# Kernel tuning notes

Measured on AMD Instinct MI355X. Metric: run time of the kernel, lower is better.

## Reference

```python
import jax, jax.numpy as jnp
import numpy as np

N = 50000      # nodes
E = 800000     # edges (before self-loops)
DIN = 256
HID = 64
HEADS = 4
DOUT = 128
NEG_SLOPE = 0.2  # PyG GATConv default leaky-relu slope


def setup_inputs() -> dict:
    key = jax.random.key(0)
    ks = jax.random.split(key, 10)
    s = 0.05
    x = jax.random.normal(ks[0], (N, DIN), jnp.float32)
    edge_index = jax.random.randint(ks[1], (2, E), 0, N, dtype=jnp.int32)
    W1 = jax.random.normal(ks[2], (DIN, HEADS * HID), jnp.float32) * s
    a1_src = jax.random.normal(ks[3], (HEADS, HID), jnp.float32) * s
    a1_dst = jax.random.normal(ks[4], (HEADS, HID), jnp.float32) * s
    b1 = jnp.zeros((HEADS * HID,), jnp.float32)
    W2 = jax.random.normal(ks[5], (HEADS * HID, DOUT), jnp.float32) * s
    a2_src = jax.random.normal(ks[6], (1, DOUT), jnp.float32) * s
    a2_dst = jax.random.normal(ks[7], (1, DOUT), jnp.float32) * s
    b2 = jnp.zeros((DOUT,), jnp.float32)
    return {"x": x, "edge_index": edge_index,
            "W1": W1, "a1_src": a1_src, "a1_dst": a1_dst, "b1": b1,
            "W2": W2, "a2_src": a2_src, "a2_dst": a2_dst, "b2": b2}


def _gat_conv(x, src, dst, W, a_src, a_dst, b, heads, concat):
    """PyG-style GATConv (self-loops already appended to src/dst)."""
    n = x.shape[0]
    h = (x @ W).reshape(n, heads, -1)               # [N, H, C]
    e_src = jnp.einsum('nhc,hc->nh', h, a_src)       # [N, H]
    e_dst = jnp.einsum('nhc,hc->nh', h, a_dst)
    logits = jax.nn.leaky_relu(e_src[src] + e_dst[dst], NEG_SLOPE)  # [E', H]
    # segment softmax over incoming edges of each dst node
    m = jax.ops.segment_max(logits, dst, num_segments=n)
    ex = jnp.exp(logits - m[dst])
    denom = jax.ops.segment_sum(ex, dst, num_segments=n)
    alpha = ex / (denom[dst] + 1e-16)                # [E', H]
    msg = alpha[:, :, None] * h[src]                 # [E', H, C]
    out = jax.ops.segment_sum(msg, dst, num_segments=n)  # [N, H, C]
    if concat:
        out = out.reshape(n, -1)
    else:
        out = out.mean(axis=1)
    return out + b


def reference(x, edge_index, W1, a1_src, a1_dst, b1, W2, a2_src, a2_dst, b2):
    n = x.shape[0]
    loop = jnp.arange(n, dtype=edge_index.dtype)
    src = jnp.concatenate([edge_index[0], loop])
    dst = jnp.concatenate([edge_index[1], loop])
    h = jax.nn.elu(_gat_conv(x, src, dst, W1, a1_src, a1_dst, b1, HEADS, True))
    h = jax.nn.elu(_gat_conv(h, src, dst, W2, a2_src, a2_dst, b2, 1, False))
    return h.mean(axis=1)  # [N]
```

## Files before the change

kernel.cpp:

```cpp
#include <hip/hip_runtime.h>
#include <math.h>

#define N_NODES 50000
#define M_PAD   50048
#define N_EDGES 800000
#define EP (N_EDGES + N_NODES)
#define DIN 256
#define HEADS 4
#define HID 64
#define F1 256
#define F2 128
#define NEG_SLOPE 0.2f
#define SCAN_NBLK ((N_NODES + 255)/256)
#define HIST_NB ((EP + 255)/256)
#define SA_NB (M_PAD*F1/4/256)
#define WT_TOT (DIN*F1 + F1*F2)
#define WT_NB ((WT_TOT + 255)/256)

typedef short bf16x8 __attribute__((ext_vector_type(8)));
typedef float f32x4  __attribute__((ext_vector_type(4)));

static __device__ __forceinline__ float leaky(float x){ return x > 0.f ? x : NEG_SLOPE*x; }
static __device__ __forceinline__ float elu_f(float x){ return x > 0.f ? x : (__expf(x)-1.f); }
static __device__ __forceinline__ float b2f(unsigned short u){ return __uint_as_float(((unsigned)u)<<16); }
static __device__ __forceinline__ unsigned short f2b(float f){
  unsigned u = __float_as_uint(f);
  return (unsigned short)((u + 0x7fffu + ((u>>16)&1u)) >> 16);
}

__global__ __launch_bounds__(256) void k_prep(const float* __restrict__ X, unsigned short* __restrict__ Ahi,
    const float* __restrict__ W1, const float* __restrict__ W2,
    unsigned short* __restrict__ Bt1, unsigned short* __restrict__ Bt2,
    const int* __restrict__ dst, int* __restrict__ counts){
  unsigned b = blockIdx.x;
  if (b < SA_NB){
    int gid = b*256 + threadIdx.x;
    size_t base = (size_t)gid*4;
    int row = (int)(base >> 8);
    ushort4 hi;
    if (row < N_NODES){
      float4 v = *(const float4*)(X + base);
      hi.x=f2b(v.x); hi.y=f2b(v.y); hi.z=f2b(v.z); hi.w=f2b(v.w);
    } else {
      hi = {0,0,0,0};
    }
    *(ushort4*)(Ahi + base) = hi;
  } else if (b < SA_NB + WT_NB){
    int t = (b - SA_NB)*256 + threadIdx.x;
    if (t < DIN*F1){
      int n = t / DIN, k = t % DIN;
      Bt1[(unsigned)n*DIN + k] = f2b(W1[(unsigned)k*F1 + n]);
    } else if (t < WT_TOT){
      int u = t - DIN*F1;
      int n = u / F1, k = u % F1;
      Bt2[(unsigned)n*F1 + k] = f2b(W2[(unsigned)k*F2 + n]);
    }
  } else {
    int e = (b - SA_NB - WT_NB)*256 + threadIdx.x;
    if (e < EP){
      int d = (e < N_EDGES) ? dst[e] : (e - N_EDGES);
      atomicAdd(&counts[d], 1);
    }
  }
}

__global__ __launch_bounds__(256) void k_scan1(const int* __restrict__ counts,
                                               int* __restrict__ exc, int* __restrict__ bsum){
  int i = blockIdx.x*256 + threadIdx.x;
  int v = (i < N_NODES) ? counts[i] : 0;
  int lane = threadIdx.x & 63, wave = threadIdx.x >> 6;
  int inc = v;
  #pragma unroll
  for (int off=1; off<64; off<<=1){
    int n = __shfl_up(inc, off);
    if (lane >= off) inc += n;
  }
  __shared__ int wsum[4];
  if (lane == 63) wsum[wave] = inc;
  __syncthreads();
  int wpre = 0;
  #pragma unroll
  for (int w=0; w<4; w++) if (w < wave) wpre += wsum[w];
  if (i < N_NODES) exc[i] = wpre + inc - v;
  if (threadIdx.x == 255) bsum[blockIdx.x] = wpre + inc;
}

__global__ __launch_bounds__(256) void k_scan3d(const int* __restrict__ exc, const int* __restrict__ bsum,
                                                const int* __restrict__ counts,
                                                int* __restrict__ offsets, int* __restrict__ cursor,
                                                int* __restrict__ dbin, int* __restrict__ bcount){
  int t = threadIdx.x;
  int lane = t & 63, wave = t >> 6;
  int v = (t < (int)blockIdx.x) ? bsum[t] : 0;
  #pragma unroll
  for (int off=1; off<64; off<<=1) v += __shfl_xor(v, off);
  __shared__ int ws[4];
  __shared__ int hh[256];
  if (lane == 0) ws[wave] = v;
  hh[t] = 0;
  __syncthreads();
  int bpref = ws[0] + ws[1] + ws[2] + ws[3];
  int i = blockIdx.x*256 + t;
  if (i < N_NODES){
    int o = exc[i] + bpref;
    offsets[i] = o;
    cursor[i] = o;
    int b = counts[i]; if (b > 255) b = 255;
    atomicAdd(&hh[b], 1);
  }
  if (i == 0) offsets[N_NODES] = EP;
  __syncthreads();
  int c = hh[t];
  bcount[(unsigned)blockIdx.x*256 + t] = c;
  if (c) atomicAdd(&dbin[t], c);
}

__global__ __launch_bounds__(256) void k_scatter_dcol(const int* __restrict__ src, const int* __restrict__ dst,
                          int* __restrict__ cursor, int* __restrict__ sorted_src, int* __restrict__ sorted_dst,
                          const int* __restrict__ dbin, const int* __restrict__ bcount, int* __restrict__ colbase){
  if (blockIdx.x < HIST_NB){
    int e = blockIdx.x*256 + threadIdx.x;
    if (e >= EP) return;
    int s, d;
    if (e < N_EDGES){ s = src[e]; d = dst[e]; } else { s = d = e - N_EDGES; }
    int pos = atomicAdd(&cursor[d], 1);
    sorted_src[pos] = s;
    sorted_dst[pos] = d;
  } else {
    int i = threadIdx.x;
    int v = dbin[i];
    int lane = i & 63, wave = i >> 6;
    int inc = v;
    #pragma unroll
    for (int off=1; off<64; off<<=1){
      int n = __shfl_up(inc, off);
      if (lane >= off) inc += n;
    }
    __shared__ int wsum[4];
    if (lane == 63) wsum[wave] = inc;
    __syncthreads();
    int wpre = 0;
    #pragma unroll
    for (int w=0; w<4; w++) if (w < wave) wpre += wsum[w];
    int run = wpre + inc - v;
    for (int blk=0; blk<SCAN_NBLK; blk++){
      colbase[(unsigned)blk*256 + i] = run;
      run += bcount[(unsigned)blk*256 + i];
    }
  }
}

__global__ __launch_bounds__(256) void k_dscatter(const int* __restrict__ counts, const int* __restrict__ colbase,
                                                  int* __restrict__ perm){
  __shared__ int h[256];
  h[threadIdx.x] = 0;
  __syncthreads();
  int i = blockIdx.x*256 + threadIdx.x;
  if (i < N_NODES){
    int b = counts[i]; if (b > 255) b = 255;
    int r = atomicAdd(&h[b], 1);
    perm[colbase[(unsigned)blockIdx.x*256 + b] + r] = i;
  }
}

__global__ __launch_bounds__(256) void k_gemm1f(
    const unsigned short* __restrict__ A, const unsigned short* __restrict__ Bt,
    const float* __restrict__ a1s, const float* __restrict__ a1d,
    unsigned short* __restrict__ Cbf, float* __restrict__ es, float* __restrict__ ed){
  const int K = 256, Nc = F1;
  int tid = threadIdx.x;
  int wave = tid>>6, lane = tid&63;
  int wc = wave;
  int row0 = blockIdx.x*64;
  int col0 = wc*64;
  int lrow = lane&15, lk = (lane>>4)*8;
  f32x4 acc[4][4] = {};
  bf16x8 aA[4], bA[4], aB[4], bB[4];
  auto LOADF = [&](bf16x8* av, bf16x8* bv, int KS){
    #pragma unroll
    for (int i=0;i<4;i++){
      av[i] = *(const bf16x8*)(A  + (unsigned)(row0 + i*16 + lrow)*K + KS + lk);
      bv[i] = *(const bf16x8*)(Bt + (unsigned)(col0 + i*16 + lrow)*K + KS + lk);
    }
  };
  auto MFMAS = [&](bf16x8* av, bf16x8* bv){
    #pragma unroll
    for (int i=0;i<4;i++)
      #pragma unroll
      for (int j=0;j<4;j++)
        acc[i][j] = __builtin_amdgcn_mfma_f32_16x16x32_bf16(av[i], bv[j], acc[i][j], 0,0,0);
  };
  LOADF(aA,bA,0);
  #pragma unroll
  for (int ks=0; ks<K; ks+=64){
    LOADF(aB,bB,ks+32);
    MFMAS(aA,bA);
    if (ks+64 < K) LOADF(aA,bA,ks+64);
    MFMAS(aB,bB);
  }
  int crow = (lane>>4)*4, ccol = lane&15;
  #pragma unroll
  for (int i=0;i<4;i++)
    #pragma unroll
    for (int j=0;j<4;j++)
      #pragma unroll
      for (int q=0;q<4;q++){
        int r = row0 + i*16 + crow + q;
        int c = col0 + j*16 + ccol;
        Cbf[(unsigned)r*Nc + c] = f2b(acc[i][j][q]);
      }
  float avs[4], avd[4];
  #pragma unroll
  for (int j=0;j<4;j++){
    avs[j] = a1s[wc*64 + j*16 + ccol];
    avd[j] = a1d[wc*64 + j*16 + ccol];
  }
  #pragma unroll
  for (int i=0;i<4;i++){
    #pragma unroll
    for (int q=0;q<4;q++){
      float ps = acc[i][0][q]*avs[0] + acc[i][1][q]*avs[1] + acc[i][2][q]*avs[2] + acc[i][3][q]*avs[3];
      float pd = acc[i][0][q]*avd[0] + acc[i][1][q]*avd[1] + acc[i][2][q]*avd[2] + acc[i][3][q]*avd[3];
      #pragma unroll
      for (int off=1; off<16; off<<=1){ ps += __shfl_xor(ps,off); pd += __shfl_xor(pd,off); }
      if ((lane&15)==0){
        int r = row0 + i*16 + crow + q;
        es[(unsigned)r*4 + wc] = ps;
        ed[(unsigned)r*4 + wc] = pd;
      }
    }
  }
}

__global__ __launch_bounds__(256) void k_gemm2(
    const unsigned short* __restrict__ A, const unsigned short* __restrict__ Bt,
    unsigned short* __restrict__ Cbf){
  const int K = 256, Nc = F2;
  int tid = threadIdx.x;
  int wave = tid>>6, lane = tid&63;
  int wr = wave>>1, wc = wave&1;
  int row0 = blockIdx.x*128 + wr*64;
  int col0 = wc*64;
  int lrow = lane&15, lk = (lane>>4)*8;
  f32x4 acc[4][4] = {};
  bf16x8 aA[4], bA[4], aB[4], bB[4];
  auto LOADF = [&](bf16x8* av, bf16x8* bv, int KS){
    #pragma unroll
    for (int i=0;i<4;i++){
      av[i] = *(const bf16x8*)(A  + (unsigned)(row0 + i*16 + lrow)*K + KS + lk);
      bv[i] = *(const bf16x8*)(Bt + (unsigned)(col0 + i*16 + lrow)*K + KS + lk);
    }
  };
  auto MFMAS = [&](bf16x8* av, bf16x8* bv){
    #pragma unroll
    for (int i=0;i<4;i++)
      #pragma unroll
      for (int j=0;j<4;j++)
        acc[i][j] = __builtin_amdgcn_mfma_f32_16x16x32_bf16(av[i], bv[j], acc[i][j], 0,0,0);
  };
  LOADF(aA,bA,0);
  #pragma unroll
  for (int ks=0; ks<K; ks+=64){
    LOADF(aB,bB,ks+32);
    MFMAS(aA,bA);
    if (ks+64 < K) LOADF(aA,bA,ks+64);
    MFMAS(aB,bB);
  }
  int crow = (lane>>4)*4, ccol = lane&15;
  #pragma unroll
  for (int i=0;i<4;i++)
    #pragma unroll
    for (int j=0;j<4;j++)
      #pragma unroll
      for (int q=0;q<4;q++){
        int r = row0 + i*16 + crow + q;
        int c = col0 + j*16 + ccol;
        Cbf[(unsigned)r*Nc + c] = f2b(acc[i][j][q]);
      }
}

__global__ __launch_bounds__(256) void k_edot2(const unsigned short* __restrict__ h2bf, const float* __restrict__ a_src,
                        const float* __restrict__ a_dst, float* __restrict__ es, float* __restrict__ ed){
  int wave=threadIdx.x>>6, lane=threadIdx.x&63;
  int n = blockIdx.x*4+wave; if (n>=N_NODES) return;
  ushort2 hv = ((const ushort2*)(h2bf + (unsigned)n*F2))[lane];
  float2 s2 = ((const float2*)a_src)[lane];
  float2 d2 = ((const float2*)a_dst)[lane];
  float h0=b2f(hv.x), h1=b2f(hv.y);
  float ps = h0*s2.x + h1*s2.y;
  float pd = h0*d2.x + h1*d2.y;
  #pragma unroll
  for (int m=1;m<64;m<<=1){ ps += __shfl_xor(ps,m); pd += __shfl_xor(pd,m); }
  if (lane==0){ es[n]=ps; ed[n]=pd; }
}

__global__ __launch_bounds__(256) void k_eexp1(const int* __restrict__ ssrc, const int* __restrict__ sdst,
                        const float* __restrict__ es, const float* __restrict__ ed,
                        float* __restrict__ ex){
  int e = blockIdx.x*256 + threadIdx.x;
  if (e >= EP) return;
  unsigned s = (unsigned)ssrc[e], d = (unsigned)sdst[e];
  float4 ev = *(const float4*)(es + s*4);
  float4 dv = *(const float4*)(ed + d*4);
  float4 o;
  o.x = __expf(leaky(ev.x+dv.x));
  o.y = __expf(leaky(ev.y+dv.y));
  o.z = __expf(leaky(ev.z+dv.z));
  o.w = __expf(leaky(ev.w+dv.w));
  *(float4*)(ex + (unsigned)e*4) = o;
}

__global__ __launch_bounds__(256) void k_eexp2(const int* __restrict__ ssrc, const int* __restrict__ sdst,
                        const float* __restrict__ es, const float* __restrict__ ed,
                        float* __restrict__ ex){
  int e = blockIdx.x*256 + threadIdx.x;
  if (e >= EP) return;
  unsigned s = (unsigned)ssrc[e], d = (unsigned)sdst[e];
  ex[e] = __expf(leaky(es[s] + ed[d]));
}

__global__ __launch_bounds__(256) void k_agg1(const unsigned short* __restrict__ h1bf, const float* __restrict__ ex1,
                       const int* __restrict__ offsets,
                       const int* __restrict__ ssrc, const int* __restrict__ perm,
                       const float* __restrict__ b1,
                       unsigned short* __restrict__ A2hi){
  int wave = threadIdx.x>>6, lane = threadIdx.x&63;
  int idx = blockIdx.x*4 + wave;
  if (idx >= M_PAD) return;
  if (idx >= N_NODES){
    ushort4 z = {0,0,0,0};
    ((ushort4*)(A2hi + (unsigned)idx*F1))[lane] = z;
    return;
  }
  int d = perm[idx];
  unsigned beg = (unsigned)offsets[d], end = (unsigned)offsets[d+1];
  unsigned deg = end - beg;
  unsigned head = (unsigned)(lane>>4);
  const ushort4* __restrict__ hb = (const ushort4*)h1bf;
  const float* __restrict__ exh = ex1 + head;
  float s0=0.f,s1=0.f,s2=0.f,s3=0.f;
  float4 acc0={0,0,0,0}, acc1={0,0,0,0}, acc2={0,0,0,0}, acc3={0,0,0,0};
  unsigned j=0;
  for (; j+4<=deg; j+=4){
    unsigned e0=beg+j;
    unsigned sn0=(unsigned)ssrc[e0], sn1=(unsigned)ssrc[e0+1], sn2=(unsigned)ssrc[e0+2], sn3=(unsigned)ssrc[e0+3];
    float x0 = exh[e0*4], x1 = exh[e0*4+4], x2 = exh[e0*4+8], x3 = exh[e0*4+12];
    ushort4 v0 = hb[sn0*64 + lane];
    ushort4 v1 = hb[sn1*64 + lane];
    ushort4 v2 = hb[sn2*64 + lane];
    ushort4 v3 = hb[sn3*64 + lane];
    s0+=x0; s1+=x1; s2+=x2; s3+=x3;
    acc0.x=fmaf(x0,b2f(v0.x),acc0.x); acc0.y=fmaf(x0,b2f(v0.y),acc0.y); acc0.z=fmaf(x0,b2f(v0.z),acc0.z); acc0.w=fmaf(x0,b2f(v0.w),acc0.w);
    acc1.x=fmaf(x1,b2f(v1.x),acc1.x); acc1.y=fmaf(x1,b2f(v1.y),acc1.y); acc1.z=fmaf(x1,b2f(v1.z),acc1.z); acc1.w=fmaf(x1,b2f(v1.w),acc1.w);
    acc2.x=fmaf(x2,b2f(v2.x),acc2.x); acc2.y=fmaf(x2,b2f(v2.y),acc2.y); acc2.z=fmaf(x2,b2f(v2.z),acc2.z); acc2.w=fmaf(x2,b2f(v2.w),acc2.w);
    acc3.x=fmaf(x3,b2f(v3.x),acc3.x); acc3.y=fmaf(x3,b2f(v3.y),acc3.y); acc3.z=fmaf(x3,b2f(v3.z),acc3.z); acc3.w=fmaf(x3,b2f(v3.w),acc3.w);
  }
  for (; j<deg; j++){
    unsigned e0=beg+j;
    unsigned sn=(unsigned)ssrc[e0];
    float x = exh[e0*4];
    ushort4 v = hb[sn*64 + lane];
    s0 += x;
    acc0.x=fmaf(x,b2f(v.x),acc0.x); acc0.y=fmaf(x,b2f(v.y),acc0.y);
    acc0.z=fmaf(x,b2f(v.z),acc0.z); acc0.w=fmaf(x,b2f(v.w),acc0.w);
  }
  float inv = 1.f/(s0+s1+s2+s3+1e-16f);
  float4 acc;
  acc.x = (acc0.x+acc1.x+acc2.x+acc3.x)*inv;
  acc.y = (acc0.y+acc1.y+acc2.y+acc3.y)*inv;
  acc.z = (acc0.z+acc1.z+acc2.z+acc3.z)*inv;
  acc.w = (acc0.w+acc1.w+acc2.w+acc3.w)*inv;
  float4 bb = *(const float4*)(b1 + lane*4);
  ushort4 hi;
  hi.x = f2b(elu_f(acc.x + bb.x));
  hi.y = f2b(elu_f(acc.y + bb.y));
  hi.z = f2b(elu_f(acc.z + bb.z));
  hi.w = f2b(elu_f(acc.w + bb.w));
  ((ushort4*)(A2hi + (unsigned)d*F1))[lane] = hi;
}

__global__ __launch_bounds__(256) void k_agg2(const unsigned short* __restrict__ h2bf, const float* __restrict__ ex2,
                       const int* __restrict__ offsets,
                       const int* __restrict__ ssrc, const int* __restrict__ perm,
                       const float* __restrict__ b2, float* __restrict__ out){
  int wave=threadIdx.x>>6, lane=threadIdx.x&63;
  int idx = blockIdx.x*4+wave; if (idx>=N_NODES) return;
  int d = perm[idx];
  unsigned beg=(unsigned)offsets[d], end=(unsigned)offsets[d+1];
  unsigned deg=end-beg;
  const ushort2* __restrict__ hb = (const ushort2*)h2bf;
  float s0=0.f,s1=0.f,s2=0.f,s3=0.f;
  float2 acc0={0,0}, acc1={0,0}, acc2={0,0}, acc3={0,0};
  unsigned j=0;
  for (; j+4<=deg; j+=4){
    unsigned e0=beg+j;
    unsigned sn0=(unsigned)ssrc[e0], sn1=(unsigned)ssrc[e0+1], sn2=(unsigned)ssrc[e0+2], sn3=(unsigned)ssrc[e0+3];
    float x0=ex2[e0], x1=ex2[e0+1], x2=ex2[e0+2], x3=ex2[e0+3];
    ushort2 v0 = hb[sn0*64 + lane];
    ushort2 v1 = hb[sn1*64 + lane];
    ushort2 v2 = hb[sn2*64 + lane];
    ushort2 v3 = hb[sn3*64 + lane];
    s0+=x0; s1+=x1; s2+=x2; s3+=x3;
    acc0.x=fmaf(x0,b2f(v0.x),acc0.x); acc0.y=fmaf(x0,b2f(v0.y),acc0.y);
    acc1.x=fmaf(x1,b2f(v1.x),acc1.x); acc1.y=fmaf(x1,b2f(v1.y),acc1.y);
    acc2.x=fmaf(x2,b2f(v2.x),acc2.x); acc2.y=fmaf(x2,b2f(v2.y),acc2.y);
    acc3.x=fmaf(x3,b2f(v3.x),acc3.x); acc3.y=fmaf(x3,b2f(v3.y),acc3.y);
  }
  for (; j<deg; j++){
    unsigned e0=beg+j;
    unsigned sn=(unsigned)ssrc[e0];
    float x = ex2[e0];
    ushort2 v = hb[sn*64 + lane];
    s0 += x;
    acc0.x=fmaf(x,b2f(v.x),acc0.x); acc0.y=fmaf(x,b2f(v.y),acc0.y);
  }
  float inv = 1.f/(s0+s1+s2+s3+1e-16f);
  float2 acc;
  acc.x = (acc0.x+acc1.x+acc2.x+acc3.x)*inv;
  acc.y = (acc0.y+acc1.y+acc2.y+acc3.y)*inv;
  float2 bb = *(const float2*)(b2 + lane*2);
  float r = elu_f(acc.x+bb.x) + elu_f(acc.y+bb.y);
  #pragma unroll
  for (int off=1;off<64;off<<=1) r += __shfl_xor(r,off);
  if (lane==0) out[d] = r * (1.f/128.f);
}

extern "C" void kernel_launch(void* const* d_in, const int* in_sizes, int n_in,
                              void* d_out, int out_size, void* d_ws, size_t ws_size,
                              hipStream_t stream) {
  const float* x   = (const float*)d_in[0];
  const int*   ei  = (const int*)d_in[1];
  const int*   esrc = ei;
  const int*   edst = ei + N_EDGES;
  const float* W1  = (const float*)d_in[2];
  const float* a1s = (const float*)d_in[3];
  const float* a1d = (const float*)d_in[4];
  const float* b1  = (const float*)d_in[5];
  const float* W2  = (const float*)d_in[6];
  const float* a2s = (const float*)d_in[7];
  const float* a2d = (const float*)d_in[8];
  const float* b2  = (const float*)d_in[9];
  float* out = (float*)d_out;

  char* ws = (char*)d_ws;
  size_t off = 0;
  auto alloc = [&](size_t bytes)->void*{ void* p = ws + off; off += (bytes + 255) & ~(size_t)255; return p; };
  unsigned short* A1hi = (unsigned short*)alloc((size_t)M_PAD*F1*2);
  unsigned short* h1bf = (unsigned short*)alloc((size_t)M_PAD*F1*2);
  unsigned short* h2bf = (unsigned short*)alloc((size_t)M_PAD*F2*2);
  unsigned short* Bt1hi= (unsigned short*)alloc((size_t)F1*DIN*2);
  unsigned short* Bt2hi= (unsigned short*)alloc((size_t)F2*F1*2);
  float* e1s   = (float*)alloc((size_t)M_PAD*HEADS*4);
  float* e1d   = (float*)alloc((size_t)M_PAD*HEADS*4);
  float* e2s   = (float*)alloc((size_t)N_NODES*4);
  float* e2d   = (float*)alloc((size_t)N_NODES*4);
  float* ex1   = (float*)alloc((size_t)EP*HEADS*4);
  float* ex2   = (float*)alloc((size_t)EP*4);
  int*   counts= (int*)alloc((size_t)N_NODES*4);
  int*   offs  = (int*)alloc((size_t)(N_NODES+1)*4);
  int*   cursor= (int*)alloc((size_t)N_NODES*4);
  int*   exc   = (int*)alloc((size_t)N_NODES*4);
  int*   bsum  = (int*)alloc((size_t)SCAN_NBLK*4);
  int*   perm  = (int*)alloc((size_t)N_NODES*4);
  int*   dbin  = (int*)alloc((size_t)256*4);
  int*   bcount= (int*)alloc((size_t)SCAN_NBLK*256*4);
  int*   colbase=(int*)alloc((size_t)SCAN_NBLK*256*4);
  int*   ssrc  = (int*)alloc((size_t)EP*4);
  int*   sdst  = (int*)alloc((size_t)EP*4);
  unsigned short* A2hi = A1hi;

  hipMemsetAsync(counts, 0, (size_t)N_NODES*4, stream);
  hipMemsetAsync(dbin, 0, (size_t)256*4, stream);
  k_prep<<<SA_NB + WT_NB + HIST_NB, 256, 0, stream>>>(x, A1hi, W1, W2, Bt1hi, Bt2hi, edst, counts);
  k_scan1<<<SCAN_NBLK, 256, 0, stream>>>(counts, exc, bsum);
  k_scan3d<<<SCAN_NBLK, 256, 0, stream>>>(exc, bsum, counts, offs, cursor, dbin, bcount);
  k_scatter_dcol<<<HIST_NB + 1, 256, 0, stream>>>(esrc, edst, cursor, ssrc, sdst, dbin, bcount, colbase);
  k_dscatter<<<SCAN_NBLK, 256, 0, stream>>>(counts, colbase, perm);

  k_gemm1f<<<M_PAD/64, 256, 0, stream>>>(A1hi, Bt1hi, a1s, a1d, h1bf, e1s, e1d);
  k_eexp1<<<HIST_NB, 256, 0, stream>>>(ssrc, sdst, e1s, e1d, ex1);
  k_agg1<<<(M_PAD+3)/4, 256, 0, stream>>>(h1bf, ex1, offs, ssrc, perm, b1, A2hi);

  k_gemm2<<<M_PAD/128, 256, 0, stream>>>(A2hi, Bt2hi, h2bf);
  k_edot2<<<(N_NODES+3)/4, 256, 0, stream>>>(h2bf, a2s, a2d, e2s, e2d);
  k_eexp2<<<HIST_NB, 256, 0, stream>>>(ssrc, sdst, e2s, e2d, ex2);
  k_agg2<<<(N_NODES+3)/4, 256, 0, stream>>>(h2bf, ex2, offs, ssrc, perm, b2, out);
}
```

Baseline: 308.6 us.

## Merge independent stages into combined launches and fuse layer-2 attention dots into GEMM

The edge scatter, degree-column scan and layer-1 GEMM now run as one launch split by block index, and the degree-sorted permutation and layer-1 edge exp run as a second combined launch. The layer-2 GEMM epilogue computes the per-node source and destination attention dot products through shared memory, which replaces the separate k_edot2 kernel. The dbin memset is moved into k_scan1. These changes remove several kernel launches and let independent work overlap, at the cost of more complex kernels whose block types have different resource needs, so occupancy may be limited by the GEMM branch.

```diff
diff --git a/kernel.cpp b/kernel.cpp
--- a/kernel.cpp
+++ b/kernel.cpp
@@ -16,6 +16,7 @@
 #define SA_NB (M_PAD*F1/4/256)
 #define WT_TOT (DIN*F1 + F1*F2)
 #define WT_NB ((WT_TOT + 255)/256)
+#define GEMM1_NB (M_PAD/64)
 
 typedef short bf16x8 __attribute__((ext_vector_type(8)));
 typedef float f32x4  __attribute__((ext_vector_type(4)));
@@ -65,7 +66,9 @@
 }
 
 __global__ __launch_bounds__(256) void k_scan1(const int* __restrict__ counts,
-                                               int* __restrict__ exc, int* __restrict__ bsum){
+                                               int* __restrict__ exc, int* __restrict__ bsum,
+                                               int* __restrict__ dbin){
+  if (blockIdx.x == 0) dbin[threadIdx.x] = 0;
   int i = blockIdx.x*256 + threadIdx.x;
   int v = (i < N_NODES) ? counts[i] : 0;
   int lane = threadIdx.x & 63, wave = threadIdx.x >> 6;
@@ -115,9 +118,13 @@
   if (c) atomicAdd(&dbin[t], c);
 }
 
-__global__ __launch_bounds__(256) void k_scatter_dcol(const int* __restrict__ src, const int* __restrict__ dst,
-                          int* __restrict__ cursor, int* __restrict__ sorted_src, int* __restrict__ sorted_dst,
-                          const int* __restrict__ dbin, const int* __restrict__ bcount, int* __restrict__ colbase){
+__global__ __launch_bounds__(256) void k_mid1(
+    const int* __restrict__ src, const int* __restrict__ dst,
+    int* __restrict__ cursor, int* __restrict__ sorted_src, int* __restrict__ sorted_dst,
+    const int* __restrict__ dbin, const int* __restrict__ bcount, int* __restrict__ colbase,
+    const unsigned short* __restrict__ A, const unsigned short* __restrict__ Bt,
+    const float* __restrict__ a1s, const float* __restrict__ a1d,
+    unsigned short* __restrict__ Cbf, float* __restrict__ es, float* __restrict__ ed){
   if (blockIdx.x < HIST_NB){
     int e = blockIdx.x*256 + threadIdx.x;
     if (e >= EP) return;
@@ -126,7 +133,9 @@
     int pos = atomicAdd(&cursor[d], 1);
     sorted_src[pos] = s;
     sorted_dst[pos] = d;
-  } else {
+    return;
+  }
+  if (blockIdx.x == HIST_NB){
     int i = threadIdx.x;
     int v = dbin[i];
     int lane = i & 63, wave = i >> 6;
@@ -147,31 +156,14 @@
       colbase[(unsigned)blk*256 + i] = run;
       run += bcount[(unsigned)blk*256 + i];
     }
-  }
-}
-
-__global__ __launch_bounds__(256) void k_dscatter(const int* __restrict__ counts, const int* __restrict__ colbase,
-                                                  int* __restrict__ perm){
-  __shared__ int h[256];
-  h[threadIdx.x] = 0;
-  __syncthreads();
-  int i = blockIdx.x*256 + threadIdx.x;
-  if (i < N_NODES){
-    int b = counts[i]; if (b > 255) b = 255;
-    int r = atomicAdd(&h[b], 1);
-    perm[colbase[(unsigned)blockIdx.x*256 + b] + r] = i;
-  }
-}
-
-__global__ __launch_bounds__(256) void k_gemm1f(
-    const unsigned short* __restrict__ A, const unsigned short* __restrict__ Bt,
-    const float* __restrict__ a1s, const float* __restrict__ a1d,
-    unsigned short* __restrict__ Cbf, float* __restrict__ es, float* __restrict__ ed){
+    return;
+  }
   const int K = 256, Nc = F1;
+  int bid = blockIdx.x - (HIST_NB + 1);
   int tid = threadIdx.x;
   int wave = tid>>6, lane = tid&63;
   int wc = wave;
-  int row0 = blockIdx.x*64;
+  int row0 = bid*64;
   int col0 = wc*64;
   int lrow = lane&15, lk = (lane>>4)*8;
   f32x4 acc[4][4] = {};
@@ -232,9 +224,39 @@
   }
 }
 
-__global__ __launch_bounds__(256) void k_gemm2(
+__global__ __launch_bounds__(256) void k_mid2(
+    const int* __restrict__ counts, const int* __restrict__ colbase, int* __restrict__ perm,
+    const int* __restrict__ ssrc, const int* __restrict__ sdst,
+    const float* __restrict__ es, const float* __restrict__ ed, float* __restrict__ ex){
+  if (blockIdx.x < SCAN_NBLK){
+    __shared__ int h[256];
+    h[threadIdx.x] = 0;
+    __syncthreads();
+    int i = blockIdx.x*256 + threadIdx.x;
+    if (i < N_NODES){
+      int b = counts[i]; if (b > 255) b = 255;
+      int r = atomicAdd(&h[b], 1);
+      perm[colbase[(unsigned)blockIdx.x*256 + b] + r] = i;
+    }
+    return;
+  }
+  int e = (blockIdx.x - SCAN_NBLK)*256 + threadIdx.x;
+  if (e >= EP) return;
+  unsigned s = (unsigned)ssrc[e], d = (unsigned)sdst[e];
+  float4 ev = *(const float4*)(es + s*4);
+  float4 dv = *(const float4*)(ed + d*4);
+  float4 o;
+  o.x = __expf(leaky(ev.x+dv.x));
+  o.y = __expf(leaky(ev.y+dv.y));
+  o.z = __expf(leaky(ev.z+dv.z));
+  o.w = __expf(leaky(ev.w+dv.w));
+  *(float4*)(ex + (unsigned)e*4) = o;
+}
+
+__global__ __launch_bounds__(256) void k_gemm2e(
     const unsigned short* __restrict__ A, const unsigned short* __restrict__ Bt,
-    unsigned short* __restrict__ Cbf){
+    const float* __restrict__ a2s, const float* __restrict__ a2d,
+    unsigned short* __restrict__ Cbf, float* __restrict__ es, float* __restrict__ ed){
   const int K = 256, Nc = F2;
   int tid = threadIdx.x;
   int wave = tid>>6, lane = tid&63;
@@ -277,37 +299,38 @@
         int c = col0 + j*16 + ccol;
         Cbf[(unsigned)r*Nc + c] = f2b(acc[i][j][q]);
       }
-}
-
-__global__ __launch_bounds__(256) void k_edot2(const unsigned short* __restrict__ h2bf, const float* __restrict__ a_src,
-                        const float* __restrict__ a_dst, float* __restrict__ es, float* __restrict__ ed){
-  int wave=threadIdx.x>>6, lane=threadIdx.x&63;
-  int n = blockIdx.x*4+wave; if (n>=N_NODES) return;
-  ushort2 hv = ((const ushort2*)(h2bf + (unsigned)n*F2))[lane];
-  float2 s2 = ((const float2*)a_src)[lane];
-  float2 d2 = ((const float2*)a_dst)[lane];
-  float h0=b2f(hv.x), h1=b2f(hv.y);
-  float ps = h0*s2.x + h1*s2.y;
-  float pd = h0*d2.x + h1*d2.y;
-  #pragma unroll
-  for (int m=1;m<64;m<<=1){ ps += __shfl_xor(ps,m); pd += __shfl_xor(pd,m); }
-  if (lane==0){ es[n]=ps; ed[n]=pd; }
-}
-
-__global__ __launch_bounds__(256) void k_eexp1(const int* __restrict__ ssrc, const int* __restrict__ sdst,
-                        const float* __restrict__ es, const float* __restrict__ ed,
-                        float* __restrict__ ex){
-  int e = blockIdx.x*256 + threadIdx.x;
-  if (e >= EP) return;
-  unsigned s = (unsigned)ssrc[e], d = (unsigned)sdst[e];
-  float4 ev = *(const float4*)(es + s*4);
-  float4 dv = *(const float4*)(ed + d*4);
-  float4 o;
-  o.x = __expf(leaky(ev.x+dv.x));
-  o.y = __expf(leaky(ev.y+dv.y));
-  o.z = __expf(leaky(ev.z+dv.z));
-  o.w = __expf(leaky(ev.w+dv.w));
-  *(float4*)(ex + (unsigned)e*4) = o;
+  __shared__ float ls[2][128];
+  __shared__ float ldd[2][128];
+  float avs[4], avd[4];
+  #pragma unroll
+  for (int j=0;j<4;j++){
+    avs[j] = a2s[col0 + j*16 + ccol];
+    avd[j] = a2d[col0 + j*16 + ccol];
+  }
+  #pragma unroll
+  for (int i=0;i<4;i++){
+    #pragma unroll
+    for (int q=0;q<4;q++){
+      float ps = acc[i][0][q]*avs[0] + acc[i][1][q]*avs[1] + acc[i][2][q]*avs[2] + acc[i][3][q]*avs[3];
+      float pd = acc[i][0][q]*avd[0] + acc[i][1][q]*avd[1] + acc[i][2][q]*avd[2] + acc[i][3][q]*avd[3];
+      #pragma unroll
+      for (int off=1; off<16; off<<=1){ ps += __shfl_xor(ps,off); pd += __shfl_xor(pd,off); }
+      if ((lane&15)==0){
+        int rb = wr*64 + i*16 + crow + q;
+        ls[wc][rb] = ps;
+        ldd[wc][rb] = pd;
+      }
+    }
+  }
+  __syncthreads();
+  int t = tid;
+  if (t < 128){
+    int n = blockIdx.x*128 + t;
+    if (n < N_NODES){
+      es[n] = ls[0][t] + ls[1][t];
+      ed[n] = ldd[0][t] + ldd[1][t];
+    }
+  }
 }
 
 __global__ __launch_bounds__(256) void k_eexp2(const int* __restrict__ ssrc, const int* __restrict__ sdst,
@@ -470,19 +493,16 @@
   unsigned short* A2hi = A1hi;
 
   hipMemsetAsync(counts, 0, (size_t)N_NODES*4, stream);
-  hipMemsetAsync(dbin, 0, (size_t)256*4, stream);
   k_prep<<<SA_NB + WT_NB + HIST_NB, 256, 0, stream>>>(x, A1hi, W1, W2, Bt1hi, Bt2hi, edst, counts);
-  k_scan1<<<SCAN_NBLK, 256, 0, stream>>>(counts, exc, bsum);
+  k_scan1<<<SCAN_NBLK, 256, 0, stream>>>(counts, exc, bsum, dbin);
   k_scan3d<<<SCAN_NBLK, 256, 0, stream>>>(exc, bsum, counts, offs, cursor, dbin, bcount);
-  k_scatter_dcol<<<HIST_NB + 1, 256, 0, stream>>>(esrc, edst, cursor, ssrc, sdst, dbin, bcount, colbase);
-  k_dscatter<<<SCAN_NBLK, 256, 0, stream>>>(counts, colbase, perm);
-
-  k_gemm1f<<<M_PAD/64, 256, 0, stream>>>(A1hi, Bt1hi, a1s, a1d, h1bf, e1s, e1d);
-  k_eexp1<<<HIST_NB, 256, 0, stream>>>(ssrc, sdst, e1s, e1d, ex1);
+  k_mid1<<<HIST_NB + 1 + GEMM1_NB, 256, 0, stream>>>(esrc, edst, cursor, ssrc, sdst,
+                                                     dbin, bcount, colbase,
+                                                     A1hi, Bt1hi, a1s, a1d, h1bf, e1s, e1d);
+  k_mid2<<<SCAN_NBLK + HIST_NB, 256, 0, stream>>>(counts, colbase, perm, ssrc, sdst, e1s, e1d, ex1);
   k_agg1<<<(M_PAD+3)/4, 256, 0, stream>>>(h1bf, ex1, offs, ssrc, perm, b1, A2hi);
 
-  k_gemm2<<<M_PAD/128, 256, 0, stream>>>(A2hi, Bt2hi, h2bf);
-  k_edot2<<<(N_NODES+3)/4, 256, 0, stream>>>(h2bf, a2s, a2d, e2s, e2d);
+  k_gemm2e<<<M_PAD/128, 256, 0, stream>>>(A2hi, Bt2hi, a2s, a2d, h2bf, e2s, e2d);
   k_eexp2<<<HIST_NB, 256, 0, stream>>>(ssrc, sdst, e2s, e2d, ex2);
   k_agg2<<<(N_NODES+3)/4, 256, 0, stream>>>(h2bf, ex2, offs, ssrc, perm, b2, out);
 }
```

After: 300.2 us. -2.7%, faster.
